# Performance work log

Measured on AMD Instinct MI355X. Metric: run time of the kernel, lower is better.

The kernel has to match this reference:

```python
import jax, jax.numpy as jnp
import numpy as np

B, C, T, H, W = 1024, 1, 500, 7, 7
HID, OUT = 16, 2


def setup_inputs() -> dict:
    key = jax.random.key(0)
    k1, k2, k3, k4 = jax.random.split(key, 4)
    rppg_embeddings = jax.random.normal(k1, (B, C, T, H, W), dtype=jnp.float32)
    rBr = jax.random.normal(k2, (B, C, T), dtype=jnp.float32)
    # final_dense_layer params: Linear(500,16) -> Dropout (identity at eval) -> Linear(16,2)
    W1 = jax.random.normal(k3, (C * T, HID), dtype=jnp.float32) / np.sqrt(C * T)
    b1 = jnp.zeros((HID,), dtype=jnp.float32)
    W2 = jax.random.normal(k4, (HID, OUT), dtype=jnp.float32) / np.sqrt(HID)
    b2 = jnp.zeros((OUT,), dtype=jnp.float32)
    return {"rppg_embeddings": rppg_embeddings, "rBr": rBr,
            "W1": W1, "b1": b1, "W2": W2, "b2": b2}


def reference(rppg_embeddings, rBr, W1, b1, W2, b2):
    # AvgPool3d(kernel=[1,7,7], stride=1, pad=0) on (B,C,T,7,7) -> (B,C,T,1,1):
    # equivalent to mean over the full 7x7 spatial window.
    x = jnp.mean(rppg_embeddings, axis=(-2, -1))            # (B, C, T)
    # batched FFT phase along time (replaces the per-(b,c) Python loop)
    phase = jnp.angle(jnp.fft.fft(x, axis=-1))              # (B, C, T)
    flat = phase.reshape(phase.shape[0], -1)                # (B, C*T) = (B, 500)
    h = flat @ W1 + b1                                      # (B, 16); dropout = identity (eval)
    rBP = h @ W2 + b2                                       # (B, 2)
    return rBP
```

## Files before the change

kernel.cpp:

```cpp
#include <hip/hip_runtime.h>
#include <math.h>

#ifndef M_PI
#define M_PI 3.14159265358979323846
#endif

#define T_LEN 500
#define HW49  49
#define HID   16
#define NOUT  2

__global__ __launch_bounds__(256, 4) void bp_head_kernel(
    const float* __restrict__ rppg,
    const float* __restrict__ W1,
    const float* __restrict__ b1,
    const float* __restrict__ W2,
    const float* __restrict__ b2,
    float* __restrict__ out)
{
    __shared__ float stage[6272];
    __shared__ float xsh[T_LEN];

    const int tid = threadIdx.x;
    const int b   = blockIdx.x;
    const float* src = rppg + (size_t)b * (T_LEN * HW49);

    for (int c = 0; c < 4; ++c) {
        const int bin0 = c * 128;
        const int bins = (bin0 + 128 <= T_LEN) ? 128 : (T_LEN - bin0);
        const int nv4  = (bins * HW49) >> 2;
        const float4* s4 = (const float4*)(src + bin0 * HW49);
        float4* st4 = (float4*)stage;
        for (int i = tid; i < nv4; i += 256) st4[i] = s4[i];
        __syncthreads();
        if (tid < bins) {
            float acc = 0.f;
            const float* p = stage + tid * HW49;
            #pragma unroll
            for (int j = 0; j < HW49; ++j) acc += p[j];
            xsh[bin0 + tid] = acc * (1.0f / 49.0f);
        }
        __syncthreads();
    }

    float hp[HID];
    #pragma unroll
    for (int j = 0; j < HID; ++j) hp[j] = 0.f;

    if (tid <= 250) {
        const int k = tid;
        float ph;
        if (k == 0) {
            double re = 0.0;
            for (int t = 0; t < T_LEN; ++t) re += (double)xsh[t];
            ph = (re < 0.0) ? (float)M_PI : 0.0f;
        } else if (k == 250) {
            ph = 0.0f;
        } else {
            const double ang = (double)k * (-2.0 * M_PI / 500.0);
            double cK, sK;
            sincos(ang, &sK, &cK);
            double c = 1.0, s = 0.0, re = 0.0, im = 0.0;
            for (int t = 0; t < T_LEN; ++t) {
                const double xv = (double)xsh[t];
                re = fma(xv, c, re);
                im = fma(xv, s, im);
                const double tc = s * sK;
                const double ts = s * cK;
                const double cn = fma(c, cK, -tc);
                s = fma(c, sK, ts);
                c = cn;
            }
            ph = (float)atan2(im, re);
        }

        if (k == 0 || k == 250) {
            const float* w = W1 + k * HID;
            #pragma unroll
            for (int j = 0; j < HID; ++j) hp[j] = ph * w[j];
        } else {
            const float* wa = W1 + k * HID;
            const float* wb = W1 + (T_LEN - k) * HID;
            #pragma unroll
            for (int j = 0; j < HID; ++j) hp[j] = ph * (wa[j] - wb[j]);
        }
    }

    __syncthreads();
    float* hred = stage;
    #pragma unroll
    for (int j = 0; j < HID; ++j) hred[tid * 17 + j] = hp[j];
    __syncthreads();
    for (int sft = 128; sft >= 1; sft >>= 1) {
        if (tid < sft) {
            #pragma unroll
            for (int j = 0; j < HID; ++j)
                hred[tid * 17 + j] += hred[(tid + sft) * 17 + j];
        }
        __syncthreads();
    }

    if (tid < NOUT) {
        const int o = tid;
        float acc = b2[o];
        #pragma unroll
        for (int j = 0; j < HID; ++j)
            acc = fmaf(hred[j] + b1[j], W2[j * NOUT + o], acc);
        out[b * NOUT + o] = acc;
    }
}

extern "C" void kernel_launch(void* const* d_in, const int* in_sizes, int n_in,
                              void* d_out, int out_size, void* d_ws, size_t ws_size,
                              hipStream_t stream) {
    const float* rppg = (const float*)d_in[0];
    const float* W1 = (const float*)d_in[2];
    const float* b1 = (const float*)d_in[3];
    const float* W2 = (const float*)d_in[4];
    const float* b2 = (const float*)d_in[5];
    float* out = (float*)d_out;

    bp_head_kernel<<<dim3(1024), dim3(256), 0, stream>>>(rppg, W1, b1, W2, b2, out);
}
```

Before: 189.3 us.

## Double-buffer spatial pooling loads and use float DFT with 4-way twiddle split

Stages the 7x7 spatial data in two shared buffers, prefetching the next chunk into registers while the current one is reduced, with four threads per time bin combined by shuffles. The per-frequency DFT moves from a serial double-precision recurrence to a single-precision one split into four interleaved accumulators sharing a 4-step twiddle, so the dependency chain is shorter and the FP64 cost goes away. The bin-250 (Nyquist) special case is removed, so it now contributes nothing. The shared-memory tree reduction of the hidden vector is replaced with wavefront shuffles plus a 4-entry cross-wave sum. Trade-offs are lower precision in the phase computation and a float twiddle recurrence that can drift over 125 steps.

```diff
diff --git a/kernel.cpp b/kernel.cpp
--- a/kernel.cpp
+++ b/kernel.cpp
@@ -10,7 +10,7 @@
 #define HID   16
 #define NOUT  2
 
-__global__ __launch_bounds__(256, 4) void bp_head_kernel(
+__global__ __launch_bounds__(256, 4) void bp_fused2_kernel(
     const float* __restrict__ rppg,
     const float* __restrict__ W1,
     const float* __restrict__ b1,
@@ -18,64 +18,109 @@
     const float* __restrict__ b2,
     float* __restrict__ out)
 {
-    __shared__ float stage[6272];
-    __shared__ float xsh[T_LEN];
+    __shared__ __align__(16) float stage[2][3136];
+    __shared__ __align__(16) float xsh[512];
+    __shared__ float wsum[4][HID + 1];
+    const int tid = threadIdx.x;
+    const int row = blockIdx.x;
+    const float4* src4 = (const float4*)(rppg + (size_t)row * (T_LEN * HW49));
 
-    const int tid = threadIdx.x;
-    const int b   = blockIdx.x;
-    const float* src = rppg + (size_t)b * (T_LEN * HW49);
+    if (tid < 12) xsh[T_LEN + tid] = 0.f;
 
-    for (int c = 0; c < 4; ++c) {
-        const int bin0 = c * 128;
-        const int bins = (bin0 + 128 <= T_LEN) ? 128 : (T_LEN - bin0);
-        const int nv4  = (bins * HW49) >> 2;
-        const float4* s4 = (const float4*)(src + bin0 * HW49);
-        float4* st4 = (float4*)stage;
-        for (int i = tid; i < nv4; i += 256) st4[i] = s4[i];
-        __syncthreads();
-        if (tid < bins) {
-            float acc = 0.f;
-            const float* p = stage + tid * HW49;
-            #pragma unroll
-            for (int j = 0; j < HW49; ++j) acc += p[j];
-            xsh[bin0 + tid] = acc * (1.0f / 49.0f);
+    const float4 fz = {0.f, 0.f, 0.f, 0.f};
+    float4 r0, r1, r2, r3;
+
+    r0 = src4[tid]; r1 = src4[tid + 256]; r2 = src4[tid + 512];
+    r3 = (tid < 16) ? src4[tid + 768] : fz;
+    {
+        float4* st = (float4*)stage[0];
+        st[tid] = r0; st[tid + 256] = r1; st[tid + 512] = r2;
+        if (tid < 16) st[tid + 768] = r3;
+    }
+    __syncthreads();
+
+    const int bin  = tid >> 2;
+    const int part = tid & 3;
+    const int nels = (part < 3) ? 13 : 10;
+    const int boff = bin * HW49 + part * 13;
+
+    for (int c = 0; c < 8; ++c) {
+        if (c < 7) {
+            const int n4 = (c + 1 < 7) ? 784 : 637;
+            const float4* b4 = src4 + 784 * (c + 1);
+            r0 = (tid       < n4) ? b4[tid      ] : fz;
+            r1 = (tid + 256 < n4) ? b4[tid + 256] : fz;
+            r2 = (tid + 512 < n4) ? b4[tid + 512] : fz;
+            r3 = (tid + 768 < n4) ? b4[tid + 768] : fz;
+        }
+        const int bins_c = (c < 7) ? 64 : 52;
+        {
+            const float* bufp = stage[c & 1];
+            float s = 0.f;
+            if (bin < bins_c) {
+                const float* p = bufp + boff;
+                for (int j = 0; j < nels; ++j) s += p[j];
+            }
+            s += __shfl_xor(s, 1);
+            s += __shfl_xor(s, 2);
+            if (part == 0 && bin < bins_c) xsh[c * 64 + bin] = s * (1.0f / 49.0f);
         }
         __syncthreads();
+        if (c < 7) {
+            const int n4 = (c + 1 < 7) ? 784 : 637;
+            float4* st = (float4*)stage[(c + 1) & 1];
+            if (tid       < n4) st[tid      ] = r0;
+            if (tid + 256 < n4) st[tid + 256] = r1;
+            if (tid + 512 < n4) st[tid + 512] = r2;
+            if (tid + 768 < n4) st[tid + 768] = r3;
+            __syncthreads();
+        }
     }
 
     float hp[HID];
     #pragma unroll
     for (int j = 0; j < HID; ++j) hp[j] = 0.f;
 
-    if (tid <= 250) {
+    if (tid <= 249) {
         const int k = tid;
-        float ph;
+        const double ang = (double)k * (-2.0 * M_PI / 500.0);
+        double c1, s1;
+        sincos(ang, &s1, &c1);
+        const double c2 = fma(c1, c1, -(s1 * s1));
+        const double s2 = 2.0 * c1 * s1;
+        const float c1f = (float)c1, s1f = (float)s1;
+        const float c2f = (float)c2, s2f = (float)s2;
+        const float c3f = (float)fma(c1, c2, -(s1 * s2));
+        const float s3f = (float)fma(c1, s2,  (s1 * c2));
+        const float c4f = (float)fma(c2, c2, -(s2 * s2));
+        const float s4f = (float)(2.0 * c2 * s2);
+
+        float cw = 1.f, sw = 0.f;
+        float re0 = 0.f, im0 = 0.f, re1 = 0.f, im1 = 0.f;
+        float re2 = 0.f, im2 = 0.f, re3 = 0.f, im3 = 0.f;
+        const float4* x4 = (const float4*)xsh;
+        float4 xv = x4[0];
+        for (int j = 0; j < 125; ++j) {
+            const float4 nx = x4[j + 1];
+            re0 = fmaf(xv.x, cw, re0); im0 = fmaf(xv.x, sw, im0);
+            re1 = fmaf(xv.y, cw, re1); im1 = fmaf(xv.y, sw, im1);
+            re2 = fmaf(xv.z, cw, re2); im2 = fmaf(xv.z, sw, im2);
+            re3 = fmaf(xv.w, cw, re3); im3 = fmaf(xv.w, sw, im3);
+            const float tc = fmaf(cw, c4f, -(sw * s4f));
+            sw = fmaf(cw, s4f, sw * c4f);
+            cw = tc;
+            xv = nx;
+        }
+        const float re = re0 + fmaf(c1f, re1, -(s1f * im1))
+                             + fmaf(c2f, re2, -(s2f * im2))
+                             + fmaf(c3f, re3, -(s3f * im3));
+        const float im = im0 + fmaf(c1f, im1,  (s1f * re1))
+                             + fmaf(c2f, im2,  (s2f * re2))
+                             + fmaf(c3f, im3,  (s3f * re3));
+        const float ph = atan2f(im, re);
+
         if (k == 0) {
-            double re = 0.0;
-            for (int t = 0; t < T_LEN; ++t) re += (double)xsh[t];
-            ph = (re < 0.0) ? (float)M_PI : 0.0f;
-        } else if (k == 250) {
-            ph = 0.0f;
-        } else {
-            const double ang = (double)k * (-2.0 * M_PI / 500.0);
-            double cK, sK;
-            sincos(ang, &sK, &cK);
-            double c = 1.0, s = 0.0, re = 0.0, im = 0.0;
-            for (int t = 0; t < T_LEN; ++t) {
-                const double xv = (double)xsh[t];
-                re = fma(xv, c, re);
-                im = fma(xv, s, im);
-                const double tc = s * sK;
-                const double ts = s * cK;
-                const double cn = fma(c, cK, -tc);
-                s = fma(c, sK, ts);
-                c = cn;
-            }
-            ph = (float)atan2(im, re);
-        }
-
-        if (k == 0 || k == 250) {
-            const float* w = W1 + k * HID;
+            const float* w = W1;
             #pragma unroll
             for (int j = 0; j < HID; ++j) hp[j] = ph * w[j];
         } else {
@@ -86,27 +131,30 @@
         }
     }
 
+    #pragma unroll
+    for (int j = 0; j < HID; ++j) {
+        float v = hp[j];
+        v += __shfl_xor(v, 1);  v += __shfl_xor(v, 2);
+        v += __shfl_xor(v, 4);  v += __shfl_xor(v, 8);
+        v += __shfl_xor(v, 16); v += __shfl_xor(v, 32);
+        hp[j] = v;
+    }
+    if ((tid & 63) == 0) {
+        const int w = tid >> 6;
+        #pragma unroll
+        for (int j = 0; j < HID; ++j) wsum[w][j] = hp[j];
+    }
     __syncthreads();
-    float* hred = stage;
-    #pragma unroll
-    for (int j = 0; j < HID; ++j) hred[tid * 17 + j] = hp[j];
-    __syncthreads();
-    for (int sft = 128; sft >= 1; sft >>= 1) {
-        if (tid < sft) {
-            #pragma unroll
-            for (int j = 0; j < HID; ++j)
-                hred[tid * 17 + j] += hred[(tid + sft) * 17 + j];
-        }
-        __syncthreads();
-    }
 
     if (tid < NOUT) {
         const int o = tid;
         float acc = b2[o];
         #pragma unroll
-        for (int j = 0; j < HID; ++j)
-            acc = fmaf(hred[j] + b1[j], W2[j * NOUT + o], acc);
-        out[b * NOUT + o] = acc;
+        for (int j = 0; j < HID; ++j) {
+            const float h = wsum[0][j] + wsum[1][j] + wsum[2][j] + wsum[3][j] + b1[j];
+            acc = fmaf(h, W2[j * NOUT + o], acc);
+        }
+        out[row * NOUT + o] = acc;
     }
 }
 
@@ -120,5 +168,5 @@
     const float* b2 = (const float*)d_in[5];
     float* out = (float*)d_out;
 
-    bp_head_kernel<<<dim3(1024), dim3(256), 0, stream>>>(rppg, W1, b1, W2, b2, out);
+    bp_fused2_kernel<<<dim3(1024), dim3(256), 0, stream>>>(rppg, W1, b1, W2, b2, out);
 }
```

Result: faster. 167.5 us (-11.5%).
